# Kernel optimization log

Hardware: AMD Instinct MI355X
Metric: run time of the kernel (lower is better)

Reference implementation:

```python
import jax, jax.numpy as jnp
import numpy as np

EMB = 1024
HEADS = 16
HEAD_SZ = EMB // HEADS
EPS = 1e-5


def _layernorm(x, g, b):
    mu = jnp.mean(x, axis=-1, keepdims=True)
    var = jnp.mean(jnp.square(x - mu), axis=-1, keepdims=True)
    return (x - mu) * jax.lax.rsqrt(var + EPS) * g + b


def setup_inputs() -> dict:
    key = jax.random.key(0)
    ks = jax.random.split(key, 12)
    s_in = 1.0 / np.sqrt(EMB)
    s_h = 1.0 / np.sqrt(4 * EMB)
    return {
        "x": jax.random.normal(ks[0], (4, 1024, EMB), jnp.float32),
        # per-head Q/K/V projections stacked: [H, EMB, HEAD_SZ], no bias
        "wq": jax.random.normal(ks[1], (HEADS, EMB, HEAD_SZ), jnp.float32) * s_in,
        "wk": jax.random.normal(ks[2], (HEADS, EMB, HEAD_SZ), jnp.float32) * s_in,
        "wv": jax.random.normal(ks[3], (HEADS, EMB, HEAD_SZ), jnp.float32) * s_in,
        "w_proj": jax.random.normal(ks[4], (EMB, EMB), jnp.float32) * s_in,
        "b_proj": jnp.zeros((EMB,), jnp.float32),
        "w1": jax.random.normal(ks[5], (EMB, 4 * EMB), jnp.float32) * s_in,
        "b1": jnp.zeros((4 * EMB,), jnp.float32),
        "w2": jax.random.normal(ks[6], (4 * EMB, EMB), jnp.float32) * s_h,
        "b2": jnp.zeros((EMB,), jnp.float32),
        "g1": jnp.ones((EMB,), jnp.float32),
        "be1": jnp.zeros((EMB,), jnp.float32),
        "g2": jnp.ones((EMB,), jnp.float32),
        "be2": jnp.zeros((EMB,), jnp.float32),
    }


def reference(x, wq, wk, wv, w_proj, b_proj, w1, b1, w2, b2, g1, be1, g2, be2):
    B, T, C = x.shape
    # --- self-attention (pre-norm) ---
    h = _layernorm(x, g1, be1)
    q = jnp.einsum("btc,hcd->bhtd", h, wq)
    k = jnp.einsum("btc,hcd->bhtd", h, wk)
    v = jnp.einsum("btc,hcd->bhtd", h, wv)
    scale = 1.0 / jnp.sqrt(jnp.asarray(HEAD_SZ, x.dtype))
    scores = jnp.einsum("bhtd,bhsd->bhts", q, k) * scale  # non-causal: SDPA called with no mask
    attn = jax.nn.softmax(scores, axis=-1)
    o = jnp.einsum("bhts,bhsd->bhtd", attn, v)
    o = o.transpose(0, 2, 1, 3).reshape(B, T, C)  # concat heads (same order as torch.cat)
    sa_out = o @ w_proj + b_proj
    x = x + sa_out
    # --- feed-forward; note ln2 applied twice, faithful to source ---
    t = _layernorm(x, g2, be2)
    t = _layernorm(t, g2, be2)
    ff = jax.nn.relu(t @ w1 + b1) @ w2 + b2
    return x + ff
```

## Files before the change

kernel.cpp:

```cpp
#include <hip/hip_runtime.h>
#include <hip/hip_bf16.h>
#include <math.h>
#include <stdint.h>

typedef __bf16 bf16_t;
typedef __bf16 bf16x4 __attribute__((ext_vector_type(4)));
typedef __bf16 bf16x8 __attribute__((ext_vector_type(8)));
typedef float floatx4 __attribute__((ext_vector_type(4)));

#define BM 128
#define BK 32

__device__ __forceinline__ size_t ftaddr(int m, int k, int KT) {
    return ((size_t)(m >> 4) * KT + (k >> 5)) * 512
         + (((k >> 3) & 3) * 16 + (m & 15)) * 8 + (k & 7);
}

__device__ __forceinline__ void gload16(const void* g, void* lds) {
    __builtin_amdgcn_global_load_lds(
        (__attribute__((address_space(1))) void*)(uintptr_t)g,
        (__attribute__((address_space(3))) void*)(uintptr_t)lds,
        16, 0, 0);
}

template<int N>
__device__ __forceinline__ void waitvm_barrier() {
    if constexpr (N == 0)       asm volatile("s_waitcnt vmcnt(0)\n\ts_barrier" ::: "memory");
    else if constexpr (N == 3)  asm volatile("s_waitcnt vmcnt(3)\n\ts_barrier" ::: "memory");
    else if constexpr (N == 4)  asm volatile("s_waitcnt vmcnt(4)\n\ts_barrier" ::: "memory");
    else if constexpr (N == 6)  asm volatile("s_waitcnt vmcnt(6)\n\ts_barrier" ::: "memory");
    else if constexpr (N == 8)  asm volatile("s_waitcnt vmcnt(8)\n\ts_barrier" ::: "memory");
    else if constexpr (N == 9)  asm volatile("s_waitcnt vmcnt(9)\n\ts_barrier" ::: "memory");
    else if constexpr (N == 12) asm volatile("s_waitcnt vmcnt(12)\n\ts_barrier" ::: "memory");
    else if constexpr (N == 16) asm volatile("s_waitcnt vmcnt(16)\n\ts_barrier" ::: "memory");
    else static_assert(N == 0, "unsupported vmcnt");
}

__device__ __forceinline__ void waitvm_barrier_rt(int n) {
    switch (n) {
    case 12: asm volatile("s_waitcnt vmcnt(12)\n\ts_barrier" ::: "memory"); break;
    case 9:  asm volatile("s_waitcnt vmcnt(9)\n\ts_barrier"  ::: "memory"); break;
    case 8:  asm volatile("s_waitcnt vmcnt(8)\n\ts_barrier"  ::: "memory"); break;
    case 6:  asm volatile("s_waitcnt vmcnt(6)\n\ts_barrier"  ::: "memory"); break;
    case 4:  asm volatile("s_waitcnt vmcnt(4)\n\ts_barrier"  ::: "memory"); break;
    case 3:  asm volatile("s_waitcnt vmcnt(3)\n\ts_barrier"  ::: "memory"); break;
    default: asm volatile("s_waitcnt vmcnt(0)\n\ts_barrier"  ::: "memory"); break;
    }
}

__global__ void prep_kernel(const float* __restrict__ wq, const float* __restrict__ wk,
                            const float* __restrict__ wv, const float* __restrict__ w_proj,
                            const float* __restrict__ w1, const float* __restrict__ w2,
                            bf16_t* __restrict__ WQKVT, bf16_t* __restrict__ WPROJT,
                            bf16_t* __restrict__ W1T, bf16_t* __restrict__ W2T,
                            const float* __restrict__ x, const float* __restrict__ g1,
                            const float* __restrict__ be1, bf16_t* __restrict__ HB)
{
    __shared__ __align__(16) char psm[33024];
    const int tid = threadIdx.x;
    if (blockIdx.x < 3072) {
        float (*tile)[65] = (float(*)[65])psm;
        const int idx = blockIdx.x;
        const float* in; bf16_t* out; int R, C, rt, ct; long nrow0;
        if (idx < 768) {
            const int z = idx >> 8;
            const int hd = (idx >> 4) & 15;
            rt = idx & 15; ct = 0; R = 1024; C = 64;
            in  = (z == 0 ? wq : z == 1 ? wk : wv) + hd * 65536;
            out = WQKVT; nrow0 = z * 1024 + hd * 64;
        } else if (idx < 1024) {
            const int t = idx - 768; rt = t & 15; ct = t >> 4; R = 1024; C = 1024;
            in = w_proj; out = WPROJT; nrow0 = 0;
        } else if (idx < 2048) {
            const int t = idx - 1024; rt = t & 15; ct = t >> 4; R = 1024; C = 4096;
            in = w1; out = W1T; nrow0 = 0;
        } else {
            const int t = idx - 2048; rt = t & 63; ct = t >> 6; R = 4096; C = 1024;
            in = w2; out = W2T; nrow0 = 0;
        }
        const int r0 = rt * 64, c0 = ct * 64;
        const int tr = tid >> 4;
        const int tc = (tid & 15) * 4;
#pragma unroll
        for (int rr = 0; rr < 4; rr++) {
            const int r = tr + rr * 16;
            const float4 v = *(const float4*)&in[(long)(r0 + r) * C + c0 + tc];
            tile[r][tc + 0] = v.x; tile[r][tc + 1] = v.y;
            tile[r][tc + 2] = v.z; tile[r][tc + 3] = v.w;
        }
        __syncthreads();
        const int KT = R >> 5;
        const int w = tid >> 6, l = tid & 63;
        const int c = l >> 4, rr2 = l & 15;
#pragma unroll
        for (int it = 0; it < 2; ++it) {
            const int t8 = it * 4 + w;
            const int kt = t8 >> 2;
            const int nb = t8 & 3;
            const long n = nrow0 + c0 + nb * 16 + rr2;
            const int k = r0 + kt * 32 + c * 8;
            bf16x8 o;
#pragma unroll
            for (int e = 0; e < 8; e++)
                o[e] = (bf16_t)tile[kt * 32 + c * 8 + e][nb * 16 + rr2];
            *(bf16x8*)&out[ftaddr((int)n, k, KT)] = o;
        }
    } else {
        bf16_t (*ybuf)[1032] = (bf16_t(*)[1032])psm;
        const int wave = tid >> 6, lane = tid & 63;
        const int rb = blockIdx.x - 3072;
        float4 gvv[4], bvv[4];
#pragma unroll
        for (int j = 0; j < 4; j++) {
            gvv[j] = ((const float4*)g1)[lane + j * 64];
            bvv[j] = ((const float4*)be1)[lane + j * 64];
        }
#pragma unroll
        for (int rr = 0; rr < 4; ++rr) {
            const int lrow = wave * 4 + rr;
            const float* xr = x + (size_t)(rb * 16 + lrow) * 1024;
            float4 v[4];
            float s = 0.f, s2 = 0.f;
#pragma unroll
            for (int j = 0; j < 4; j++) {
                v[j] = ((const float4*)xr)[lane + j * 64];
                s  += v[j].x + v[j].y + v[j].z + v[j].w;
                s2 += v[j].x * v[j].x + v[j].y * v[j].y + v[j].z * v[j].z + v[j].w * v[j].w;
            }
#pragma unroll
            for (int off = 32; off >= 1; off >>= 1) {
                s  += __shfl_xor(s, off);
                s2 += __shfl_xor(s2, off);
            }
            const float mu = s * (1.0f / 1024.0f);
            const float rs = rsqrtf(fmaxf(s2 * (1.0f / 1024.0f) - mu * mu, 0.f) + 1e-5f);
#pragma unroll
            for (int j = 0; j < 4; j++) {
                bf16x4 o;
                o[0] = (bf16_t)((v[j].x - mu) * rs * gvv[j].x + bvv[j].x);
                o[1] = (bf16_t)((v[j].y - mu) * rs * gvv[j].y + bvv[j].y);
                o[2] = (bf16_t)((v[j].z - mu) * rs * gvv[j].z + bvv[j].z);
                o[3] = (bf16_t)((v[j].w - mu) * rs * gvv[j].w + bvv[j].w);
                *(bf16x4*)&ybuf[lrow][(lane + j * 64) * 4] = o;
            }
        }
        __syncthreads();
        bf16_t* outBase = HB + (size_t)rb * 32 * 512;
#pragma unroll
        for (int it = 0; it < 8; ++it) {
            const int s = it * 256 + tid;
            const int kt = s >> 6, c = (s >> 4) & 3, rr2 = s & 15;
            const bf16x8 val = *(const bf16x8*)&ybuf[rr2][kt * 32 + c * 8];
            *(bf16x8*)&outBase[(size_t)s * 8] = val;
        }
    }
}

__global__ void ln2x_kernel(const float* __restrict__ x, const float* __restrict__ g,
                            const float* __restrict__ b, bf16_t* __restrict__ outb)
{
    __shared__ __align__(16) bf16_t ybuf[16][1032];
    const int tid = threadIdx.x, wave = tid >> 6, lane = tid & 63;
    const int rb = blockIdx.x;
    float4 gvv[4], bvv[4];
#pragma unroll
    for (int j = 0; j < 4; j++) {
        gvv[j] = ((const float4*)g)[lane + j * 64];
        bvv[j] = ((const float4*)b)[lane + j * 64];
    }
#pragma unroll
    for (int rr = 0; rr < 4; ++rr) {
        const int lrow = wave * 4 + rr;
        const float* xr = x + (size_t)(rb * 16 + lrow) * 1024;
        float4 v[4];
        float s = 0.f, s2 = 0.f;
#pragma unroll
        for (int j = 0; j < 4; j++) {
            v[j] = ((const float4*)xr)[lane + j * 64];
            s  += v[j].x + v[j].y + v[j].z + v[j].w;
            s2 += v[j].x * v[j].x + v[j].y * v[j].y + v[j].z * v[j].z + v[j].w * v[j].w;
        }
#pragma unroll
        for (int off = 32; off >= 1; off >>= 1) {
            s  += __shfl_xor(s, off);
            s2 += __shfl_xor(s2, off);
        }
        float mu = s * (1.0f / 1024.0f);
        float rs = rsqrtf(fmaxf(s2 * (1.0f / 1024.0f) - mu * mu, 0.f) + 1e-5f);
        s = 0.f; s2 = 0.f;
#pragma unroll
        for (int j = 0; j < 4; j++) {
            v[j].x = (v[j].x - mu) * rs * gvv[j].x + bvv[j].x;
            v[j].y = (v[j].y - mu) * rs * gvv[j].y + bvv[j].y;
            v[j].z = (v[j].z - mu) * rs * gvv[j].z + bvv[j].z;
            v[j].w = (v[j].w - mu) * rs * gvv[j].w + bvv[j].w;
            s  += v[j].x + v[j].y + v[j].z + v[j].w;
            s2 += v[j].x * v[j].x + v[j].y * v[j].y + v[j].z * v[j].z + v[j].w * v[j].w;
        }
#pragma unroll
        for (int off = 32; off >= 1; off >>= 1) {
            s  += __shfl_xor(s, off);
            s2 += __shfl_xor(s2, off);
        }
        mu = s * (1.0f / 1024.0f);
        rs = rsqrtf(fmaxf(s2 * (1.0f / 1024.0f) - mu * mu, 0.f) + 1e-5f);
#pragma unroll
        for (int j = 0; j < 4; j++) {
            bf16x4 o;
            o[0] = (bf16_t)((v[j].x - mu) * rs * gvv[j].x + bvv[j].x);
            o[1] = (bf16_t)((v[j].y - mu) * rs * gvv[j].y + bvv[j].y);
            o[2] = (bf16_t)((v[j].z - mu) * rs * gvv[j].z + bvv[j].z);
            o[3] = (bf16_t)((v[j].w - mu) * rs * gvv[j].w + bvv[j].w);
            *(bf16x4*)&ybuf[lrow][(lane + j * 64) * 4] = o;
        }
    }
    __syncthreads();
    bf16_t* outBase = outb + (size_t)rb * 32 * 512;
#pragma unroll
    for (int it = 0; it < 8; ++it) {
        const int s = it * 256 + tid;
        const int kt = s >> 6, c = (s >> 4) & 3, rr2 = s & 15;
        const bf16x8 val = *(const bf16x8*)&ybuf[rr2][kt * 32 + c * 8];
        *(bf16x8*)&outBase[(size_t)s * 8] = val;
    }
}

template<int EPI, int BNt, int DEPTH>
__global__ __launch_bounds__(256, (BNt == 64 ? 3 : 2))
void gemm_bt(const bf16_t* __restrict__ A, const bf16_t* __restrict__ Bt,
             const int K,
             const float* __restrict__ bias, const float* __restrict__ resid,
             float* __restrict__ outf, bf16_t* __restrict__ outb,
             bf16_t* __restrict__ aux1, bf16_t* __restrict__ aux2,
             const int Nout)
{
    constexpr int NFRAG = BNt / 16;
    constexpr int LPS = (BNt == 128) ? 4 : 3;
    constexpr int ASZ = DEPTH * 8 * 512;
    constexpr int BSZ = DEPTH * NFRAG * 512;
    __shared__ __align__(16) bf16_t smem[ASZ + BSZ];
    bf16_t* Asb = smem;
    bf16_t* Bsb = smem + ASZ;
    const int tid  = threadIdx.x;
    const int wave = tid >> 6, lane = tid & 63;
    const int bm = blockIdx.x * BM, bn = blockIdx.y * BNt;
    const int KT = K >> 5;

    floatx4 acc[2][NFRAG];
#pragma unroll
    for (int i = 0; i < 2; i++)
#pragma unroll
        for (int j = 0; j < NFRAG; j++) acc[i][j] = (floatx4){0.f, 0.f, 0.f, 0.f};

    const bf16_t* gA0 = A + ((size_t)(bm / 16 + wave * 2 + 0) * KT) * 512 + lane * 8;
    const bf16_t* gA1 = A + ((size_t)(bm / 16 + wave * 2 + 1) * KT) * 512 + lane * 8;
    const int lA0 = (wave * 2 + 0) * 512;
    const int lA1 = (wave * 2 + 1) * 512;

    const bf16_t* gB0;
    const bf16_t* gB1 = nullptr;
    int lB0, lB1 = 0;
    if (BNt == 128) {
        gB0 = Bt + ((size_t)(bn / 16 + wave * 2 + 0) * KT) * 512 + lane * 8;
        gB1 = Bt + ((size_t)(bn / 16 + wave * 2 + 1) * KT) * 512 + lane * 8;
        lB0 = (wave * 2 + 0) * 512;
        lB1 = (wave * 2 + 1) * 512;
    } else {
        gB0 = Bt + ((size_t)(bn / 16 + wave) * KT) * 512 + lane * 8;
        lB0 = wave * 512;
    }

    auto stage = [&](int t, int bu) {
        const size_t off = (size_t)t * 512;
        gload16(gA0 + off, Asb + bu * 4096 + lA0);
        gload16(gA1 + off, Asb + bu * 4096 + lA1);
        gload16(gB0 + off, Bsb + bu * (NFRAG * 512) + lB0);
        if (BNt == 128) gload16(gB1 + off, Bsb + bu * (NFRAG * 512) + lB1);
    };

    auto compute = [&](int bu) {
        bf16x8 af[2], bfv[NFRAG];
#pragma unroll
        for (int i = 0; i < 2; i++)
            af[i] = *(const bf16x8*)&Asb[bu * 4096 + (wave * 2 + i) * 512 + lane * 8];
#pragma unroll
        for (int j = 0; j < NFRAG; j++)
            bfv[j] = *(const bf16x8*)&Bsb[bu * (NFRAG * 512) + j * 512 + lane * 8];
#pragma unroll
        for (int i = 0; i < 2; i++)
#pragma unroll
            for (int j = 0; j < NFRAG; j++)
                acc[i][j] = __builtin_amdgcn_mfma_f32_16x16x32_bf16(af[i], bfv[j], acc[i][j], 0, 0, 0);
    };

    const int NT = K / BK;
#pragma unroll
    for (int i = 0; i < DEPTH - 1; ++i) stage(i, i);
    int bu = 0;
    for (int t = 0; t <= NT - DEPTH; ++t) {
        waitvm_barrier<LPS * (DEPTH - 2)>();
        stage(t + DEPTH - 1, bu == 0 ? DEPTH - 1 : bu - 1);
        compute(bu);
        bu = (bu + 1 == DEPTH) ? 0 : bu + 1;
    }
#pragma unroll
    for (int j = DEPTH - 2; j >= 0; --j) {
        waitvm_barrier_rt(LPS * j);
        compute(bu);
        bu = (bu + 1 == DEPTH) ? 0 : bu + 1;
    }

    const int er = (lane >> 4) * 4, ec = lane & 15;
    if (EPI == 0 && bn >= 2048) {
        __syncthreads();
        bf16_t* scr = smem;
#pragma unroll
        for (int i = 0; i < 2; i++)
#pragma unroll
            for (int j = 0; j < NFRAG; j++)
#pragma unroll
                for (int r = 0; r < 4; r++)
                    scr[(j * 16 + ec) * 136 + wave * 32 + i * 16 + er + r] =
                        (bf16_t)acc[i][j][r];
        __syncthreads();
        const int bq = bm >> 10, tmod = bm & 1023, h0 = (bn - 2048) >> 6;
#pragma unroll
        for (int it = 0; it < 8; ++it) {
            const int c = it * 256 + tid;
            const int dl = c >> 4, t16 = c & 15;
            const bf16x8 val = *(const bf16x8*)&scr[dl * 136 + t16 * 8];
            const int h = h0 + (dl >> 6), dd = dl & 63;
            *(bf16x8*)&aux2[(size_t)((bq * 16 + h) * 64 + dd) * 1024 + tmod + t16 * 8] = val;
        }
        return;
    }
#pragma unroll
    for (int i = 0; i < 2; i++) {
#pragma unroll
        for (int j = 0; j < NFRAG; j++) {
            const int col = bn + j * 16 + ec;
#pragma unroll
            for (int r = 0; r < 4; r++) {
                const int row = bm + wave * 32 + i * 16 + er + r;
                const float v = acc[i][j][r];
                if (EPI == 0) {
                    const int b = row >> 10, t = row & 1023;
                    if (col < 1024) {
                        const int h = col >> 6, d = col & 63;
                        outb[(size_t)((b * 16 + h) * 1024 + t) * 64 + d] = (bf16_t)v;
                    } else {
                        const int c2 = col - 1024, h = c2 >> 6, d = c2 & 63;
                        aux1[(size_t)((b * 16 + h) * 1024 + t) * 64 + d] = (bf16_t)v;
                    }
                } else if (EPI == 1 || EPI == 3) {
                    const size_t idx = (size_t)row * Nout + col;
                    outf[idx] = v + bias[col] + resid[idx];
                } else if (EPI == 2) {
                    outb[ftaddr(row, col, Nout >> 5)] = (bf16_t)fmaxf(v + bias[col], 0.f);
                }
            }
        }
    }
}

__global__ __launch_bounds__(256, 4)
void attn_kernel(const bf16_t* __restrict__ Q, const bf16_t* __restrict__ Kg,
                 const bf16_t* __restrict__ Vt, bf16_t* __restrict__ Og)
{
    __shared__ __align__(16) bf16_t Ks[2][4096];
    __shared__ __align__(16) bf16_t Vs[2][4096];
    __shared__ __align__(16) bf16_t Ps[4][1024];
    const int tid = threadIdx.x, wave = tid >> 6, lane = tid & 63;
    const int lin = blockIdx.x + (blockIdx.y << 4);
    const int xcd = lin & 7, idx = lin >> 3;
    const int bh = xcd * 8 + (idx >> 4);
    const int qt = idx & 15;
    const int b = bh >> 4, h = bh & 15;
    const int q0 = qt * 64 + wave * 16;
    const bf16_t* Qb = Q + (size_t)bh * 65536;
    const char* Kb = (const char*)(Kg + (size_t)bh * 65536);
    const char* Vb = (const char*)(Vt + (size_t)bh * 65536);
    const int fr = lane & 15, g = lane >> 4, fk = g * 8;

    const bf16x8 qf0 = *(const bf16x8*)&Qb[(size_t)(q0 + fr) * 64 + fk];
    const bf16x8 qf1 = *(const bf16x8*)&Qb[(size_t)(q0 + fr) * 64 + 32 + fk];

    floatx4 o[4];
#pragma unroll
    for (int dt = 0; dt < 4; dt++) o[dt] = (floatx4){0.f, 0.f, 0.f, 0.f};
    float lsum[4] = {0.f, 0.f, 0.f, 0.f};
    bf16_t* pw = &Ps[wave][0];
    const float sscale = 0.125f * 1.44269504088896f;

    auto stage = [&](int s0, int bu) {
#pragma unroll
        for (int t = 0; t < 2; t++) {
            const int j = wave * 2 + t;
            gload16(Kb + (size_t)(s0 + lane) * 128 + j * 16, &Ks[bu][j * 512]);
            gload16(Vb + (size_t)lane * 2048 + (size_t)s0 * 2 + j * 16, &Vs[bu][j * 512]);
        }
    };

    stage(0, 0);
    int bu = 0;
    for (int it = 0; it < 16; ++it) {
        __syncthreads();
        if (it < 15) stage((it + 1) * 64, bu ^ 1);
        const bf16_t* Kl = Ks[bu];
        const bf16_t* Vl = Vs[bu];

        floatx4 sacc[4];
#pragma unroll
        for (int ss = 0; ss < 4; ss++) sacc[ss] = (floatx4){0.f, 0.f, 0.f, 0.f};
        __builtin_amdgcn_s_setprio(1);
#pragma unroll
        for (int ss = 0; ss < 4; ss++) {
#pragma unroll
            for (int c = 0; c < 2; c++) {
                const int ch = c * 4 + g;
                const bf16x8 qf = (c == 0) ? qf0 : qf1;
                const bf16x8 kf = *(const bf16x8*)&Kl[ch * 512 + (ss * 16 + fr) * 8];
                sacc[ss] = __builtin_amdgcn_mfma_f32_16x16x32_bf16(qf, kf, sacc[ss], 0, 0, 0);
            }
        }
        __builtin_amdgcn_s_setprio(0);
#pragma unroll
        for (int ss = 0; ss < 2; ss++) {
#pragma unroll
            for (int r = 0; r < 4; r++) {
                const float p = __builtin_amdgcn_exp2f(sacc[ss][r] * sscale);
                lsum[r] += p;
                const int q = g * 4 + r;
                pw[(ss * 2 + (fr >> 3)) * 128 + q * 8 + (fr & 7)] = (bf16_t)p;
            }
        }
        asm volatile("s_waitcnt lgkmcnt(0)" ::: "memory");
#pragma unroll
        for (int ss = 2; ss < 4; ss++) {
#pragma unroll
            for (int r = 0; r < 4; r++) {
                const float p = __builtin_amdgcn_exp2f(sacc[ss][r] * sscale);
                lsum[r] += p;
                const int q = g * 4 + r;
                pw[(ss * 2 + (fr >> 3)) * 128 + q * 8 + (fr & 7)] = (bf16_t)p;
            }
        }
        {
            const int ch = g;
            const bf16x8 pf = *(const bf16x8*)&pw[ch * 128 + fr * 8];
            __builtin_amdgcn_s_setprio(1);
#pragma unroll
            for (int dt = 0; dt < 4; dt++) {
                const bf16x8 vf = *(const bf16x8*)&Vl[ch * 512 + (dt * 16 + fr) * 8];
                o[dt] = __builtin_amdgcn_mfma_f32_16x16x32_bf16(pf, vf, o[dt], 0, 0, 0);
            }
            __builtin_amdgcn_s_setprio(0);
        }
        asm volatile("s_waitcnt lgkmcnt(0)" ::: "memory");
        {
            const int ch = 4 + g;
            const bf16x8 pf = *(const bf16x8*)&pw[ch * 128 + fr * 8];
            __builtin_amdgcn_s_setprio(1);
#pragma unroll
            for (int dt = 0; dt < 4; dt++) {
                const bf16x8 vf = *(const bf16x8*)&Vl[ch * 512 + (dt * 16 + fr) * 8];
                o[dt] = __builtin_amdgcn_mfma_f32_16x16x32_bf16(pf, vf, o[dt], 0, 0, 0);
            }
            __builtin_amdgcn_s_setprio(0);
        }
        asm volatile("" ::: "memory");
        bu ^= 1;
    }
#pragma unroll
    for (int r = 0; r < 4; r++) {
        float l = lsum[r];
        l += __shfl_xor(l, 1);
        l += __shfl_xor(l, 2);
        l += __shfl_xor(l, 4);
        l += __shfl_xor(l, 8);
        lsum[r] = 1.0f / l;
    }
    const int tq = q0 + g * 4;
#pragma unroll
    for (int dt = 0; dt < 4; dt++) {
#pragma unroll
        for (int r = 0; r < 4; r++) {
            const int m = b * 1024 + tq + r;
            const int k = h * 64 + dt * 16 + fr;
            Og[ftaddr(m, k, 32)] = (bf16_t)(o[dt][r] * lsum[r]);
        }
    }
}

extern "C" void kernel_launch(void* const* d_in, const int* in_sizes, int n_in,
                              void* d_out, int out_size, void* d_ws, size_t ws_size,
                              hipStream_t stream)
{
    const float* x      = (const float*)d_in[0];
    const float* wq     = (const float*)d_in[1];
    const float* wk     = (const float*)d_in[2];
    const float* wv     = (const float*)d_in[3];
    const float* w_proj = (const float*)d_in[4];
    const float* b_proj = (const float*)d_in[5];
    const float* w1     = (const float*)d_in[6];
    const float* b1     = (const float*)d_in[7];
    const float* w2     = (const float*)d_in[8];
    const float* b2     = (const float*)d_in[9];
    const float* g1     = (const float*)d_in[10];
    const float* be1    = (const float*)d_in[11];
    const float* g2     = (const float*)d_in[12];
    const float* be2    = (const float*)d_in[13];
    float* out = (float*)d_out;
    char* ws = (char*)d_ws;

    bf16_t* WQKVT = (bf16_t*)(ws + 0x0000000);
    bf16_t* WPROJT= (bf16_t*)(ws + 0x0600000);
    bf16_t* W1T   = (bf16_t*)(ws + 0x0800000);
    bf16_t* W2T   = (bf16_t*)(ws + 0x1000000);
    bf16_t* HB    = (bf16_t*)(ws + 0x1800000);
    bf16_t* Qb    = (bf16_t*)(ws + 0x2000000);
    bf16_t* Kb    = (bf16_t*)(ws + 0x2800000);
    bf16_t* Vtb   = (bf16_t*)(ws + 0x3000000);
    bf16_t* AO    = (bf16_t*)(ws + 0x3800000);
    float*  X2    = (float*)(ws + 0x4000000);
    bf16_t* TB    = (bf16_t*)(ws + 0x2800000);
    bf16_t* FF1B  = (bf16_t*)(ws + 0x5000000);

    dim3 blk(256);
    prep_kernel<<<3328, blk, 0, stream>>>(wq, wk, wv, w_proj, w1, w2,
                                          WQKVT, WPROJT, W1T, W2T,
                                          x, g1, be1, HB);
    gemm_bt<0, 128, 5><<<dim3(32, 24), blk, 0, stream>>>(HB, WQKVT, 1024, nullptr, nullptr,
                                                         nullptr, Qb, Kb, Vtb, 3072);
    attn_kernel<<<dim3(16, 64), blk, 0, stream>>>(Qb, Kb, Vtb, AO);
    gemm_bt<1, 64, 4><<<dim3(32, 16), blk, 0, stream>>>(AO, WPROJT, 1024, b_proj, x,
                                                        X2, nullptr, nullptr, nullptr, 1024);
    ln2x_kernel<<<256, blk, 0, stream>>>(X2, g2, be2, TB);
    gemm_bt<2, 128, 5><<<dim3(32, 32), blk, 0, stream>>>(TB, W1T, 1024, b1, nullptr,
                                                         nullptr, FF1B, nullptr, nullptr, 4096);
    gemm_bt<3, 64, 4><<<dim3(32, 16), blk, 0, stream>>>(FF1B, W2T, 4096, b2, X2,
                                                        out, nullptr, nullptr, nullptr, 1024);
}
```

Measured before the change: 303.9 us.

## Use 2x2 wave grid with 64x64 per-wave tiles in all GEMMs

```diff
diff --git a/kernel.cpp b/kernel.cpp
--- a/kernel.cpp
+++ b/kernel.cpp
@@ -26,11 +26,8 @@
 template<int N>
 __device__ __forceinline__ void waitvm_barrier() {
     if constexpr (N == 0)       asm volatile("s_waitcnt vmcnt(0)\n\ts_barrier" ::: "memory");
-    else if constexpr (N == 3)  asm volatile("s_waitcnt vmcnt(3)\n\ts_barrier" ::: "memory");
     else if constexpr (N == 4)  asm volatile("s_waitcnt vmcnt(4)\n\ts_barrier" ::: "memory");
-    else if constexpr (N == 6)  asm volatile("s_waitcnt vmcnt(6)\n\ts_barrier" ::: "memory");
     else if constexpr (N == 8)  asm volatile("s_waitcnt vmcnt(8)\n\ts_barrier" ::: "memory");
-    else if constexpr (N == 9)  asm volatile("s_waitcnt vmcnt(9)\n\ts_barrier" ::: "memory");
     else if constexpr (N == 12) asm volatile("s_waitcnt vmcnt(12)\n\ts_barrier" ::: "memory");
     else if constexpr (N == 16) asm volatile("s_waitcnt vmcnt(16)\n\ts_barrier" ::: "memory");
     else static_assert(N == 0, "unsupported vmcnt");
@@ -39,11 +36,8 @@
 __device__ __forceinline__ void waitvm_barrier_rt(int n) {
     switch (n) {
     case 12: asm volatile("s_waitcnt vmcnt(12)\n\ts_barrier" ::: "memory"); break;
-    case 9:  asm volatile("s_waitcnt vmcnt(9)\n\ts_barrier"  ::: "memory"); break;
     case 8:  asm volatile("s_waitcnt vmcnt(8)\n\ts_barrier"  ::: "memory"); break;
-    case 6:  asm volatile("s_waitcnt vmcnt(6)\n\ts_barrier"  ::: "memory"); break;
     case 4:  asm volatile("s_waitcnt vmcnt(4)\n\ts_barrier"  ::: "memory"); break;
-    case 3:  asm volatile("s_waitcnt vmcnt(3)\n\ts_barrier"  ::: "memory"); break;
     default: asm volatile("s_waitcnt vmcnt(0)\n\ts_barrier"  ::: "memory"); break;
     }
 }
@@ -225,8 +219,8 @@
     }
 }
 
-template<int EPI, int BNt, int DEPTH>
-__global__ __launch_bounds__(256, (BNt == 64 ? 3 : 2))
+template<int EPI, int DEPTH>
+__global__ __launch_bounds__(256, 2)
 void gemm_bt(const bf16_t* __restrict__ A, const bf16_t* __restrict__ Bt,
              const int K,
              const float* __restrict__ bias, const float* __restrict__ resid,
@@ -234,62 +228,51 @@
              bf16_t* __restrict__ aux1, bf16_t* __restrict__ aux2,
              const int Nout)
 {
-    constexpr int NFRAG = BNt / 16;
-    constexpr int LPS = (BNt == 128) ? 4 : 3;
+    constexpr int LPS = 4;
     constexpr int ASZ = DEPTH * 8 * 512;
-    constexpr int BSZ = DEPTH * NFRAG * 512;
+    constexpr int BSZ = DEPTH * 8 * 512;
     __shared__ __align__(16) bf16_t smem[ASZ + BSZ];
     bf16_t* Asb = smem;
     bf16_t* Bsb = smem + ASZ;
     const int tid  = threadIdx.x;
     const int wave = tid >> 6, lane = tid & 63;
-    const int bm = blockIdx.x * BM, bn = blockIdx.y * BNt;
+    const int wr = wave >> 1, wc = wave & 1;
+    const int bm = blockIdx.x * BM, bn = blockIdx.y * 128;
     const int KT = K >> 5;
 
-    floatx4 acc[2][NFRAG];
-#pragma unroll
-    for (int i = 0; i < 2; i++)
-#pragma unroll
-        for (int j = 0; j < NFRAG; j++) acc[i][j] = (floatx4){0.f, 0.f, 0.f, 0.f};
+    floatx4 acc[4][4];
+#pragma unroll
+    for (int i = 0; i < 4; i++)
+#pragma unroll
+        for (int j = 0; j < 4; j++) acc[i][j] = (floatx4){0.f, 0.f, 0.f, 0.f};
 
     const bf16_t* gA0 = A + ((size_t)(bm / 16 + wave * 2 + 0) * KT) * 512 + lane * 8;
     const bf16_t* gA1 = A + ((size_t)(bm / 16 + wave * 2 + 1) * KT) * 512 + lane * 8;
+    const bf16_t* gB0 = Bt + ((size_t)(bn / 16 + wave * 2 + 0) * KT) * 512 + lane * 8;
+    const bf16_t* gB1 = Bt + ((size_t)(bn / 16 + wave * 2 + 1) * KT) * 512 + lane * 8;
     const int lA0 = (wave * 2 + 0) * 512;
     const int lA1 = (wave * 2 + 1) * 512;
-
-    const bf16_t* gB0;
-    const bf16_t* gB1 = nullptr;
-    int lB0, lB1 = 0;
-    if (BNt == 128) {
-        gB0 = Bt + ((size_t)(bn / 16 + wave * 2 + 0) * KT) * 512 + lane * 8;
-        gB1 = Bt + ((size_t)(bn / 16 + wave * 2 + 1) * KT) * 512 + lane * 8;
-        lB0 = (wave * 2 + 0) * 512;
-        lB1 = (wave * 2 + 1) * 512;
-    } else {
-        gB0 = Bt + ((size_t)(bn / 16 + wave) * KT) * 512 + lane * 8;
-        lB0 = wave * 512;
-    }
 
     auto stage = [&](int t, int bu) {
         const size_t off = (size_t)t * 512;
         gload16(gA0 + off, Asb + bu * 4096 + lA0);
         gload16(gA1 + off, Asb + bu * 4096 + lA1);
-        gload16(gB0 + off, Bsb + bu * (NFRAG * 512) + lB0);
-        if (BNt == 128) gload16(gB1 + off, Bsb + bu * (NFRAG * 512) + lB1);
+        gload16(gB0 + off, Bsb + bu * 4096 + lA0);
+        gload16(gB1 + off, Bsb + bu * 4096 + lA1);
     };
 
     auto compute = [&](int bu) {
-        bf16x8 af[2], bfv[NFRAG];
-#pragma unroll
-        for (int i = 0; i < 2; i++)
-            af[i] = *(const bf16x8*)&Asb[bu * 4096 + (wave * 2 + i) * 512 + lane * 8];
-#pragma unroll
-        for (int j = 0; j < NFRAG; j++)
-            bfv[j] = *(const bf16x8*)&Bsb[bu * (NFRAG * 512) + j * 512 + lane * 8];
-#pragma unroll
-        for (int i = 0; i < 2; i++)
-#pragma unroll
-            for (int j = 0; j < NFRAG; j++)
+        bf16x8 af[4], bfv[4];
+#pragma unroll
+        for (int i = 0; i < 4; i++)
+            af[i] = *(const bf16x8*)&Asb[bu * 4096 + (wr * 4 + i) * 512 + lane * 8];
+#pragma unroll
+        for (int j = 0; j < 4; j++)
+            bfv[j] = *(const bf16x8*)&Bsb[bu * 4096 + (wc * 4 + j) * 512 + lane * 8];
+#pragma unroll
+        for (int i = 0; i < 4; i++)
+#pragma unroll
+            for (int j = 0; j < 4; j++)
                 acc[i][j] = __builtin_amdgcn_mfma_f32_16x16x32_bf16(af[i], bfv[j], acc[i][j], 0, 0, 0);
     };
 
@@ -315,12 +298,12 @@
         __syncthreads();
         bf16_t* scr = smem;
 #pragma unroll
-        for (int i = 0; i < 2; i++)
-#pragma unroll
-            for (int j = 0; j < NFRAG; j++)
+        for (int i = 0; i < 4; i++)
+#pragma unroll
+            for (int j = 0; j < 4; j++)
 #pragma unroll
                 for (int r = 0; r < 4; r++)
-                    scr[(j * 16 + ec) * 136 + wave * 32 + i * 16 + er + r] =
+                    scr[((wc * 4 + j) * 16 + ec) * 136 + (wr * 4 + i) * 16 + er + r] =
                         (bf16_t)acc[i][j][r];
         __syncthreads();
         const int bq = bm >> 10, tmod = bm & 1023, h0 = (bn - 2048) >> 6;
@@ -335,13 +318,13 @@
         return;
     }
 #pragma unroll
-    for (int i = 0; i < 2; i++) {
-#pragma unroll
-        for (int j = 0; j < NFRAG; j++) {
-            const int col = bn + j * 16 + ec;
+    for (int i = 0; i < 4; i++) {
+#pragma unroll
+        for (int j = 0; j < 4; j++) {
+            const int col = bn + (wc * 4 + j) * 16 + ec;
 #pragma unroll
             for (int r = 0; r < 4; r++) {
-                const int row = bm + wave * 32 + i * 16 + er + r;
+                const int row = bm + (wr * 4 + i) * 16 + er + r;
                 const float v = acc[i][j][r];
                 if (EPI == 0) {
                     const int b = row >> 10, t = row & 1023;
@@ -530,14 +513,14 @@
     prep_kernel<<<3328, blk, 0, stream>>>(wq, wk, wv, w_proj, w1, w2,
                                           WQKVT, WPROJT, W1T, W2T,
                                           x, g1, be1, HB);
-    gemm_bt<0, 128, 5><<<dim3(32, 24), blk, 0, stream>>>(HB, WQKVT, 1024, nullptr, nullptr,
-                                                         nullptr, Qb, Kb, Vtb, 3072);
+    gemm_bt<0, 5><<<dim3(32, 24), blk, 0, stream>>>(HB, WQKVT, 1024, nullptr, nullptr,
+                                                    nullptr, Qb, Kb, Vtb, 3072);
     attn_kernel<<<dim3(16, 64), blk, 0, stream>>>(Qb, Kb, Vtb, AO);
-    gemm_bt<1, 64, 4><<<dim3(32, 16), blk, 0, stream>>>(AO, WPROJT, 1024, b_proj, x,
-                                                        X2, nullptr, nullptr, nullptr, 1024);
+    gemm_bt<1, 5><<<dim3(32, 8), blk, 0, stream>>>(AO, WPROJT, 1024, b_proj, x,
+                                                   X2, nullptr, nullptr, nullptr, 1024);
     ln2x_kernel<<<256, blk, 0, stream>>>(X2, g2, be2, TB);
-    gemm_bt<2, 128, 5><<<dim3(32, 32), blk, 0, stream>>>(TB, W1T, 1024, b1, nullptr,
-                                                         nullptr, FF1B, nullptr, nullptr, 4096);
-    gemm_bt<3, 64, 4><<<dim3(32, 16), blk, 0, stream>>>(FF1B, W2T, 4096, b2, X2,
-                                                        out, nullptr, nullptr, nullptr, 1024);
-}
+    gemm_bt<2, 5><<<dim3(32, 32), blk, 0, stream>>>(TB, W1T, 1024, b1, nullptr,
+                                                    nullptr, FF1B, nullptr, nullptr, 4096);
+    gemm_bt<3, 5><<<dim3(32, 8), blk, 0, stream>>>(FF1B, W2T, 4096, b2, X2,
+                                                   out, nullptr, nullptr, nullptr, 1024);
+}
```

Result: no change. 299.3 us (-1.5%).
